# Kernel tuning notes

Hardware: AMD Instinct MI355X
Metric: run time of the kernel (lower is better)

## Reference

```python
import jax, jax.numpy as jnp
import numpy as np

N, E, G = 25600, 409600, 128   # nodes, edges, graphs
IN, H, C = 200, 4, 64          # raw feat dim, heads, hidden_channels
IN2 = 2 * IN                   # after NaN-mask concat
BN_EPS = 1e-5

def _glorot(key, shape):
    lim = float(np.sqrt(6.0 / (shape[0] + shape[-1])))
    return jax.random.uniform(key, shape, jnp.float32, -lim, lim)

def setup_inputs():
    key = jax.random.key(0)
    k = iter(jax.random.split(key, 40))
    inp = {
        "x": jax.random.normal(next(k), (N, IN), jnp.float32),
        "edge_index": jax.random.randint(next(k), (2, E), 0, N, jnp.int32),
        "edge_attr": jax.random.normal(next(k), (E, 1), jnp.float32),
        "batch": jnp.repeat(jnp.arange(G, dtype=jnp.int32), N // G),
    }
    dims = [(IN2, H, C), (H * C, H, C), (H * C, 1, C)]
    for i, (din, h, c) in enumerate(dims):
        inp[f"W{i}"] = _glorot(next(k), (din, h * c))
        inp[f"as{i}"] = _glorot(next(k), (h, c))
        inp[f"ad{i}"] = _glorot(next(k), (h, c))
        inp[f"We{i}"] = _glorot(next(k), (1, h * c))
        inp[f"ae{i}"] = _glorot(next(k), (h, c))
        inp[f"b{i}"] = jnp.zeros((h * c,), jnp.float32)
    inp["bn_g"] = jnp.ones((H * C,), jnp.float32)
    inp["bn_b"] = jnp.zeros((H * C,), jnp.float32)
    inp["bn_m"] = jnp.zeros((H * C,), jnp.float32)
    inp["bn_v"] = jnp.ones((H * C,), jnp.float32)
    inp["cw1"] = _glorot(next(k), (C, C))
    inp["cb1"] = jnp.zeros((C,), jnp.float32)
    inp["cw2"] = _glorot(next(k), (C, 2))
    inp["cb2"] = jnp.zeros((2,), jnp.float32)
    return inp

def _gat(x, src, dst, ea, W, att_s, att_d, We, att_e, b, heads, ch):
    """PyG GATConv (edge_dim=1, add_self_loops=True, fill_value='mean', concat=True)."""
    n = x.shape[0]
    # self-loop edge_attr = mean of incoming edge_attr per destination node
    cnt = jax.ops.segment_sum(jnp.ones((ea.shape[0], 1), ea.dtype), dst, n)
    loop_ea = jax.ops.segment_sum(ea, dst, n) / jnp.maximum(cnt, 1.0)
    idx = jnp.arange(n, dtype=src.dtype)
    src = jnp.concatenate([src, idx])
    dst = jnp.concatenate([dst, idx])
    ea = jnp.concatenate([ea, loop_ea], axis=0)
    h = (x @ W).reshape(n, heads, ch)                      # [N,H,C]
    a_s = jnp.einsum('nhc,hc->nh', h, att_s)
    a_d = jnp.einsum('nhc,hc->nh', h, att_d)
    a_e = jnp.einsum('ehc,hc->eh', (ea @ We).reshape(-1, heads, ch), att_e)
    alpha = jax.nn.leaky_relu(a_s[src] + a_d[dst] + a_e, 0.2)   # [E',H]
    # segment softmax over destination neighborhoods
    m = jax.ops.segment_max(alpha, dst, n)
    ex = jnp.exp(alpha - m[dst])
    z = jax.ops.segment_sum(ex, dst, n)
    alpha = ex / (z[dst] + 1e-16)
    out = jax.ops.segment_sum(h[src] * alpha[:, :, None], dst, n)  # [N,H,C]
    return out.reshape(n, heads * ch) + b

def reference(x, edge_index, edge_attr, batch,
              W0, as0, ad0, We0, ae0, b0,
              W1, as1, ad1, We1, ae1, b1,
              W2, as2, ad2, We2, ae2, b2,
              bn_g, bn_b, bn_m, bn_v, cw1, cb1, cw2, cb2):
    nan_mask = jnp.isnan(x).astype(x.dtype)
    x = jnp.concatenate([jnp.nan_to_num(x), nan_mask], axis=-1)   # [N, 2*IN]
    edge_attr = jnp.nan_to_num(edge_attr)
    src, dst = edge_index[0], edge_index[1]
    for (W, a_s, a_d, We, a_e, b) in [(W0, as0, ad0, We0, ae0, b0),
                                      (W1, as1, ad1, We1, ae1, b1)]:
        x = _gat(x, src, dst, edge_attr, W, a_s, a_d, We, a_e, b, H, C)
        x = (x - bn_m) / jnp.sqrt(bn_v + BN_EPS) * bn_g + bn_b    # eval-mode BN
        x = jax.nn.relu(x)                                        # dropout = identity (eval)
    x = _gat(x, src, dst, edge_attr, W2, as2, ad2, We2, ae2, b2, 1, C)
    # global mean pool over graphs
    cnt = jax.ops.segment_sum(jnp.ones((x.shape[0], 1), x.dtype), batch, G)
    g = jax.ops.segment_sum(x, batch, G) / jnp.maximum(cnt, 1.0)  # [G, C]
    hdn = jax.nn.gelu(g @ cw1 + cb1, approximate=False)
    return hdn @ cw2 + cb2                                        # [G, 2]
```

## Files before the change

kernel.cpp:

```cpp
#include <hip/hip_runtime.h>
#include <hip/hip_bf16.h>

static const int kN  = 25600;
static const int kE  = 409600;
static const int kG  = 128;
static const int kNPG = 200;
static const int kIN = 200;
static const int kIN2 = 400;
static const int kMD = 64;
#define BN_EPS_ 1e-5f

typedef __attribute__((ext_vector_type(8))) short short8;
typedef __attribute__((ext_vector_type(4))) ushort us4;
typedef __attribute__((ext_vector_type(4))) float f32x4;

__device__ __forceinline__ float bu(ushort u) {
  union { float f; unsigned u32; } x; x.u32 = ((unsigned)u) << 16; return x.f;
}
__device__ __forceinline__ ushort f2u(float v) {
  __hip_bfloat16 t = __float2bfloat16(v);
  return *(ushort*)&t;
}
__device__ __forceinline__ float wredSum(float v) {
#pragma unroll
  for (int off = 1; off < 64; off <<= 1) v += __shfl_xor(v, off, 64);
  return v;
}
__device__ __forceinline__ float lrelu(float a) { return (a > 0.f) ? a : 0.2f * a; }

__global__ void k_pre(const float* __restrict__ x, ushort* __restrict__ x2,
                      const float* __restrict__ W0, ushort* __restrict__ Wt0,
                      const float* __restrict__ W1, ushort* __restrict__ Wt1,
                      const float* __restrict__ W2, ushort* __restrict__ Wt2,
                      const float* __restrict__ We0, const float* __restrict__ ae0,
                      const float* __restrict__ We1, const float* __restrict__ ae1,
                      const float* __restrict__ We2, const float* __restrict__ ae2,
                      float* __restrict__ wed,
                      const int* __restrict__ ei, const float* __restrict__ ea,
                      int2* __restrict__ epk, int* __restrict__ deg) {
  int b = blockIdx.x, tid = threadIdx.x;
  if (b < 5000) {
    int i4 = (b * 256 + tid) * 4;
    int n = i4 / kIN, j = i4 - n * kIN;
    float4 v = *(const float4*)&x[i4];
    ushort o0[4], o1[4];
    float vv[4] = {v.x, v.y, v.z, v.w};
#pragma unroll
    for (int q = 0; q < 4; q++) {
      bool bad = (vv[q] != vv[q]);
      o0[q] = f2u(bad ? 0.f : vv[q]);
      o1[q] = f2u(bad ? 1.f : 0.f);
    }
    *(us4*)&x2[(size_t)n * kIN2 + j] = *(us4*)o0;
    *(us4*)&x2[(size_t)n * kIN2 + kIN + j] = *(us4*)o1;
    return;
  }
  int pb = b - 5000;
  if (pb >= 723) {
    int e = (pb - 723) * 256 + tid;
    int d = ei[kE + e];
    int s = ei[e];
    float v = ea[e];
    if (v != v) v = 0.f;
    int slot = atomicAdd(&deg[d], 1);
    if (slot < kMD) {
      int2 rec; rec.x = s; rec.y = __float_as_int(v);
      epk[(size_t)d * kMD + slot] = rec;
    }
    return;
  }
  if (pb >= 720) {
    int l = pb - 720;
    const float* We = (l == 0) ? We0 : (l == 1) ? We1 : We2;
    const float* ae = (l == 0) ? ae0 : (l == 1) ? ae1 : ae2;
    int n = (l == 2) ? 64 : 256;
    float v = (tid < n) ? We[tid] * ae[tid] : 0.f;
    v = wredSum(v);
    if ((tid & 63) == 0 && tid < n) wed[l * 4 + (tid >> 6)] = v;
    return;
  }
  int i = pb * 256 + tid;
  if (i < 102400) {
    int n = i / kIN2, k = i - n * kIN2;
    Wt0[(size_t)n * kIN2 + k] = f2u(W0[(size_t)k * 256 + n]);
  } else if (i < 102400 + 65536) {
    int j = i - 102400;
    int n = j >> 8, k = j & 255;
    Wt1[(size_t)n * 256 + k] = f2u(W1[(size_t)k * 256 + n]);
  } else {
    int j = i - 102400 - 65536;
    int n = j >> 8, k = j & 255;
    Wt2[(size_t)n * 256 + k] = f2u(W2[(size_t)k * 64 + n]);
  }
}

#define GBK 64
#define GPAD 72

template <int BN, int MT>
__global__ __launch_bounds__(256) void k_gemm_f(const ushort* __restrict__ A,
                                                const ushort* __restrict__ Bt,
                                                ushort* __restrict__ C,
                                                const float* __restrict__ as_g,
                                                const float* __restrict__ ad_g,
                                                float* __restrict__ a_sg,
                                                float* __restrict__ a_dg, int K) {
  constexpr int MI = (BN == 256) ? (MT / 16) : 1;
  constexpr int H = (BN == 256) ? 4 : 1;
  __shared__ ushort As[MT * GPAD];
  __shared__ ushort Bs[BN * GPAD];
  int tid = threadIdx.x;
  int lane = tid & 63, w = tid >> 6;
  int l15 = lane & 15, l4 = lane >> 4;
  int row0 = blockIdx.y * MT;
  int wr = (BN == 256) ? 0 : (w * 16);
  int wc = (BN == 256) ? (w * 64) : 0;
  f32x4 acc[MI][4] = {};
  int ach = tid & 7, arow = tid >> 3;

  for (int kt = 0; kt < K; kt += GBK) {
    __syncthreads();
#pragma unroll
    for (int p = 0; p < MT / 32; p++) {
      int r = p * 32 + arow;
      int kg = kt + ach * 8;
      short8 v = {0, 0, 0, 0, 0, 0, 0, 0};
      if (kg < K) v = *(const short8*)&A[(size_t)(row0 + r) * K + kg];
      *(short8*)&As[r * GPAD + ach * 8] = v;
    }
#pragma unroll
    for (int p = 0; p < BN / 32; p++) {
      int r = p * 32 + arow;
      int kg = kt + ach * 8;
      short8 v = {0, 0, 0, 0, 0, 0, 0, 0};
      if (kg < K) v = *(const short8*)&Bt[(size_t)r * K + kg];
      *(short8*)&Bs[r * GPAD + ach * 8] = v;
    }
    __syncthreads();
#pragma unroll
    for (int kk = 0; kk < 2; kk++) {
      short8 af[MI], bf[4];
#pragma unroll
      for (int mi = 0; mi < MI; mi++)
        af[mi] = *(const short8*)&As[(wr + mi * 16 + l15) * GPAD + kk * 32 + l4 * 8];
#pragma unroll
      for (int ni = 0; ni < 4; ni++)
        bf[ni] = *(const short8*)&Bs[(wc + ni * 16 + l15) * GPAD + kk * 32 + l4 * 8];
#pragma unroll
      for (int mi = 0; mi < MI; mi++)
#pragma unroll
        for (int ni = 0; ni < 4; ni++)
          acc[mi][ni] = __builtin_amdgcn_mfma_f32_16x16x32_bf16(af[mi], bf[ni],
                                                                acc[mi][ni], 0, 0, 0);
    }
  }
#pragma unroll
  for (int mi = 0; mi < MI; mi++) {
    int rbase = row0 + wr + mi * 16 + l4 * 4;
#pragma unroll
    for (int ni = 0; ni < 4; ni++) {
      int col = wc + ni * 16 + l15;
#pragma unroll
      for (int r = 0; r < 4; r++)
        C[(size_t)(rbase + r) * BN + col] = f2u(acc[mi][ni][r]);
    }
  }
  float asv[4], adv[4];
#pragma unroll
  for (int ni = 0; ni < 4; ni++) {
    asv[ni] = as_g[wc + ni * 16 + l15];
    adv[ni] = ad_g[wc + ni * 16 + l15];
  }
  int hh = (BN == 256) ? w : 0;
#pragma unroll
  for (int mi = 0; mi < MI; mi++) {
#pragma unroll
    for (int r = 0; r < 4; r++) {
      float ps = 0.f, pd = 0.f;
#pragma unroll
      for (int ni = 0; ni < 4; ni++) {
        ps += acc[mi][ni][r] * asv[ni];
        pd += acc[mi][ni][r] * adv[ni];
      }
#pragma unroll
      for (int off = 1; off < 16; off <<= 1) {
        ps += __shfl_xor(ps, off, 64);
        pd += __shfl_xor(pd, off, 64);
      }
      if (l15 == 0) {
        int row = row0 + wr + mi * 16 + l4 * 4 + r;
        a_sg[row * H + hh] = ps;
        a_dg[row * H + hh] = pd;
      }
    }
  }
}

__global__ __launch_bounds__(256) void k_agg4(
    const ushort* __restrict__ hbuf, const int2* __restrict__ epk,
    const int* __restrict__ deg, const float* __restrict__ a_s,
    const float* __restrict__ a_d, const float* __restrict__ wed,
    const float* __restrict__ bias, const float* __restrict__ bng,
    const float* __restrict__ bnb, const float* __restrict__ bnm,
    const float* __restrict__ bnv, ushort* __restrict__ xout) {
  __shared__ float lds_w[4][kMD][4];
  __shared__ int   lds_s[4][kMD];
  __shared__ float lds_m[4][4][2];
  int tid = threadIdx.x;
  int w = tid >> 6, lane = tid & 63;
  int d = blockIdx.x * 4 + w;
  const int2* rp = &epk[(size_t)d * kMD];
  int dgt = deg[d];
  int dg = min(dgt, kMD);

  int h1 = lane & 3, slot0 = lane >> 2;
  float adh1 = a_d[d * 4 + h1];
  float wdh1 = wed[h1];
  float szp = 0.f, seap = 0.f;
  for (int t = 0; t < dg; t += 16) {
    int slot = t + slot0;
    float wv = 0.f, ev = 0.f;
    if (slot < dg) {
      int2 rec = rp[slot];
      ev = __int_as_float(rec.y);
      float asv = a_s[rec.x * 4 + h1];
      wv = __expf(lrelu(asv + adh1 + ev * wdh1));
      lds_w[w][slot][h1] = wv;
      if (h1 == 0) lds_s[w][slot] = rec.x;
    }
    szp += wv;
    seap += (h1 == 0) ? ev : 0.f;
  }
#pragma unroll
  for (int off = 4; off < 64; off <<= 1) {
    szp  += __shfl_xor(szp, off, 64);
    seap += __shfl_xor(seap, off, 64);
  }
  float sea = __shfl(seap, lane & 0x3C, 64);
  float lea = sea / fmaxf((float)dgt, 1.f);
  float selfw1 = __expf(lrelu(a_s[d * 4 + h1] + adh1 + lea * wdh1));
  float szh = szp + selfw1;
  if (slot0 == 0) {
    lds_m[w][h1][0] = 1.f / (szh + 1e-16f);
    lds_m[w][h1][1] = selfw1;
  }

  int h2 = lane >> 4;
  int c0 = lane * 4;
  float a0 = 0.f, a1 = 0.f, a2 = 0.f, a3 = 0.f;
  int k = 0;
  for (; k + 8 <= dg; k += 8) {
    int s8[8]; float w8[8];
#pragma unroll
    for (int j = 0; j < 8; j++) {
      s8[j] = lds_s[w][k + j];
      w8[j] = lds_w[w][k + j][h2];
    }
    ushort4 v8[8];
#pragma unroll
    for (int j = 0; j < 8; j++)
      v8[j] = *(const ushort4*)&hbuf[(size_t)s8[j] * 256 + c0];
#pragma unroll
    for (int j = 0; j < 8; j++) {
      a0 += w8[j] * bu(v8[j].x); a1 += w8[j] * bu(v8[j].y);
      a2 += w8[j] * bu(v8[j].z); a3 += w8[j] * bu(v8[j].w);
    }
  }
  for (; k < dg; k++) {
    int s0 = lds_s[w][k];
    float w0 = lds_w[w][k][h2];
    ushort4 v0 = *(const ushort4*)&hbuf[(size_t)s0 * 256 + c0];
    a0 += w0 * bu(v0.x); a1 += w0 * bu(v0.y);
    a2 += w0 * bu(v0.z); a3 += w0 * bu(v0.w);
  }
  float winv = lds_m[w][h2][0];
  float sw   = lds_m[w][h2][1];
  {
    ushort4 v0 = *(const ushort4*)&hbuf[(size_t)d * 256 + c0];
    a0 += sw * bu(v0.x); a1 += sw * bu(v0.y);
    a2 += sw * bu(v0.z); a3 += sw * bu(v0.w);
  }

  float4 bi = *(const float4*)&bias[c0];
  a0 = a0 * winv + bi.x; a1 = a1 * winv + bi.y;
  a2 = a2 * winv + bi.z; a3 = a3 * winv + bi.w;
  float4 g4 = *(const float4*)&bng[c0], b4 = *(const float4*)&bnb[c0];
  float4 m4 = *(const float4*)&bnm[c0], v4 = *(const float4*)&bnv[c0];
  a0 = fmaxf((a0 - m4.x) * rsqrtf(v4.x + BN_EPS_) * g4.x + b4.x, 0.f);
  a1 = fmaxf((a1 - m4.y) * rsqrtf(v4.y + BN_EPS_) * g4.y + b4.y, 0.f);
  a2 = fmaxf((a2 - m4.z) * rsqrtf(v4.z + BN_EPS_) * g4.z + b4.z, 0.f);
  a3 = fmaxf((a3 - m4.w) * rsqrtf(v4.w + BN_EPS_) * g4.w + b4.w, 0.f);
  ushort4 o = make_ushort4(f2u(a0), f2u(a1), f2u(a2), f2u(a3));
  *(ushort4*)&xout[(size_t)d * 256 + c0] = o;
}

__global__ __launch_bounds__(256) void k_agg1(
    const ushort* __restrict__ hbuf, const int2* __restrict__ epk,
    const int* __restrict__ deg, const float* __restrict__ a_s,
    const float* __restrict__ a_d, const float* __restrict__ wed,
    const float* __restrict__ bias, float* __restrict__ xout) {
  __shared__ float lds_w[4][kMD];
  __shared__ int   lds_s[4][kMD];
  int tid = threadIdx.x;
  int w = tid >> 6, lane = tid & 63;
  int d = blockIdx.x * 4 + w;
  const int2* rp = &epk[(size_t)d * kMD];
  int dgt = deg[d];
  int dg = min(dgt, kMD);
  float adh = a_d[d];
  float wdh = wed[0];

  float wv = 0.f, ev = 0.f;
  if (lane < dg) {
    int2 rec = rp[lane];
    ev = __int_as_float(rec.y);
    wv = __expf(lrelu(a_s[rec.x] + adh + ev * wdh));
    lds_w[w][lane] = wv;
    lds_s[w][lane] = rec.x;
  }
  float szp = wv, seap = ev;
#pragma unroll
  for (int off = 1; off < 64; off <<= 1) {
    szp  += __shfl_xor(szp, off, 64);
    seap += __shfl_xor(seap, off, 64);
  }
  float lea = seap / fmaxf((float)dgt, 1.f);
  float selfw = __expf(lrelu(a_s[d] + adh + lea * wdh));
  float winv = 1.f / (szp + selfw + 1e-16f);

  float acc = 0.f;
  int k = 0;
  for (; k + 8 <= dg; k += 8) {
    int s8[8]; float w8[8];
#pragma unroll
    for (int j = 0; j < 8; j++) {
      s8[j] = lds_s[w][k + j];
      w8[j] = lds_w[w][k + j];
    }
    ushort v8[8];
#pragma unroll
    for (int j = 0; j < 8; j++) v8[j] = hbuf[(size_t)s8[j] * 64 + lane];
#pragma unroll
    for (int j = 0; j < 8; j++) acc += w8[j] * bu(v8[j]);
  }
  for (; k < dg; k++) {
    acc += lds_w[w][k] * bu(hbuf[(size_t)lds_s[w][k] * 64 + lane]);
  }
  acc += selfw * bu(hbuf[(size_t)d * 64 + lane]);
  acc = acc * winv + bias[lane];
  xout[(size_t)d * 64 + lane] = acc;
}

__global__ void k_poolhead(const float* __restrict__ xin,
                           const float* __restrict__ cw1, const float* __restrict__ cb1,
                           const float* __restrict__ cw2, const float* __restrict__ cb2,
                           float* __restrict__ out) {
  __shared__ float part[4][64];
  __shared__ float gb[64], hb[64];
  int g = blockIdx.x, tid = threadIdx.x;
  int c = tid & 63, w = tid >> 6;
  float acc = 0.f;
  size_t base = (size_t)g * kNPG * 64;
  for (int n = w; n < kNPG; n += 4) acc += xin[base + (size_t)n * 64 + c];
  part[w][c] = acc;
  __syncthreads();
  if (tid < 64) {
    float s = (part[0][c] + part[1][c]) + (part[2][c] + part[3][c]);
    gb[c] = s * (1.f / kNPG);
  }
  __syncthreads();
  if (tid < 64) {
    float s = cb1[c];
#pragma unroll 8
    for (int i = 0; i < 64; i++) s += gb[i] * cw1[i * 64 + c];
    s = 0.5f * s * (1.f + erff(s * 0.70710678118654752f));
    hb[c] = s;
  }
  __syncthreads();
  if (tid < 2) {
    float o = cb2[tid];
    for (int i = 0; i < 64; i++) o += hb[i] * cw2[i * 2 + tid];
    out[g * 2 + tid] = o;
  }
}


extern "C" void kernel_launch(void* const* d_in, const int* in_sizes, int n_in,
                              void* d_out, int out_size, void* d_ws, size_t ws_size,
                              hipStream_t stream) {
  (void)in_sizes; (void)n_in; (void)out_size; (void)ws_size;
  const float* x  = (const float*)d_in[0];
  const int* ei   = (const int*)d_in[1];
  const float* ea = (const float*)d_in[2];
  const float *W[3], *as_[3], *ad_[3], *We[3], *ae[3], *bi[3];
  for (int l = 0; l < 3; l++) {
    W[l]   = (const float*)d_in[4 + l * 6 + 0];
    as_[l] = (const float*)d_in[4 + l * 6 + 1];
    ad_[l] = (const float*)d_in[4 + l * 6 + 2];
    We[l]  = (const float*)d_in[4 + l * 6 + 3];
    ae[l]  = (const float*)d_in[4 + l * 6 + 4];
    bi[l]  = (const float*)d_in[4 + l * 6 + 5];
  }
  const float* bng = (const float*)d_in[22];
  const float* bnb = (const float*)d_in[23];
  const float* bnm = (const float*)d_in[24];
  const float* bnv = (const float*)d_in[25];
  const float* cw1 = (const float*)d_in[26];
  const float* cb1 = (const float*)d_in[27];
  const float* cw2 = (const float*)d_in[28];
  const float* cb2 = (const float*)d_in[29];

  char* p = (char*)d_ws;
  auto alloc = [&](size_t bytes) -> void* {
    void* r = (void*)p;
    p += (bytes + 255) & ~(size_t)255;
    return r;
  };
  ushort* x2b   = (ushort*)alloc((size_t)kN * kIN2 * 2);
  ushort* hbufb = (ushort*)alloc((size_t)kN * 256 * 2);
  ushort* xbA   = (ushort*)alloc((size_t)kN * 256 * 2);
  ushort* xbB   = (ushort*)alloc((size_t)kN * 256 * 2);
  float*  fbuf  = (float*)alloc((size_t)kN * 64 * 4);
  ushort* Wt0   = (ushort*)alloc((size_t)kIN2 * 256 * 2);
  ushort* Wt1   = (ushort*)alloc((size_t)256 * 256 * 2);
  ushort* Wt2   = (ushort*)alloc((size_t)256 * 64 * 2);
  float* a_s    = (float*)alloc((size_t)kN * 4 * 4);
  float* a_d    = (float*)alloc((size_t)kN * 4 * 4);
  int2* epk     = (int2*)alloc((size_t)kN * kMD * 8);
  float* wed    = (float*)alloc(256);
  int* deg      = (int*)alloc((size_t)kN * 4);

  hipMemsetAsync(deg, 0, (size_t)kN * 4, stream);
  k_pre<<<5000 + 720 + 3 + 1600, 256, 0, stream>>>(
      x, x2b, W[0], Wt0, W[1], Wt1, W[2], Wt2, We[0], ae[0], We[1], ae[1],
      We[2], ae[2], wed, ei, ea, epk, deg);
  dim3 gg64m(1, kN / 64);
  k_gemm_f<256, 64><<<gg64m, 256, 0, stream>>>(x2b, Wt0, hbufb, as_[0], ad_[0],
                                               a_s, a_d, kIN2);
  k_agg4<<<kN / 4, 256, 0, stream>>>(hbufb, epk, deg, a_s, a_d,
                                     &wed[0], bi[0], bng, bnb, bnm, bnv, xbA);
  k_gemm_f<256, 64><<<gg64m, 256, 0, stream>>>(xbA, Wt1, hbufb, as_[1], ad_[1],
                                               a_s, a_d, 256);
  k_agg4<<<kN / 4, 256, 0, stream>>>(hbufb, epk, deg, a_s, a_d,
                                     &wed[4], bi[1], bng, bnb, bnm, bnv, xbB);
  dim3 gg64(1, kN / 64);
  k_gemm_f<64, 64><<<gg64, 256, 0, stream>>>(xbB, Wt2, hbufb, as_[2], ad_[2],
                                             a_s, a_d, 256);
  k_agg1<<<kN / 4, 256, 0, stream>>>(hbufb, epk, deg, a_s, a_d,
                                     &wed[8], bi[2], fbuf);
  k_poolhead<<<kG, 256, 0, stream>>>(fbuf, cw1, cb1, cw2, cb2, (float*)d_out);
}
```

Before: 299.3 us.

## Use direct global-to-LDS loads with XOR swizzle, fuse pooling into aggregation

```diff
diff --git a/kernel.cpp b/kernel.cpp
--- a/kernel.cpp
+++ b/kernel.cpp
@@ -7,6 +7,7 @@
 static const int kNPG = 200;
 static const int kIN = 200;
 static const int kIN2 = 400;
+static const int kK0 = 448;
 static const int kMD = 64;
 #define BN_EPS_ 1e-5f
 
@@ -27,6 +28,10 @@
   return v;
 }
 __device__ __forceinline__ float lrelu(float a) { return (a > 0.f) ? a : 0.2f * a; }
+
+#define GLOAD16(g, l) __builtin_amdgcn_global_load_lds( \
+    (const __attribute__((address_space(1))) unsigned int*)(g), \
+    (__attribute__((address_space(3))) unsigned int*)(l), 16, 0, 0)
 
 __global__ void k_pre(const float* __restrict__ x, ushort* __restrict__ x2,
                       const float* __restrict__ W0, ushort* __restrict__ Wt0,
@@ -51,11 +56,26 @@
       o0[q] = f2u(bad ? 0.f : vv[q]);
       o1[q] = f2u(bad ? 1.f : 0.f);
     }
-    *(us4*)&x2[(size_t)n * kIN2 + j] = *(us4*)o0;
-    *(us4*)&x2[(size_t)n * kIN2 + kIN + j] = *(us4*)o1;
+    *(us4*)&x2[(size_t)n * kK0 + j] = *(us4*)o0;
+    *(us4*)&x2[(size_t)n * kK0 + kIN + j] = *(us4*)o1;
     return;
   }
   int pb = b - 5000;
+  if (pb >= 2323) {
+    int idx = (pb - 2323) * 256 + tid;
+    short8 z = {0, 0, 0, 0, 0, 0, 0, 0};
+    if (idx < 153600) {
+      int row = idx / 6, c = idx - row * 6;
+      *(short8*)&x2[(size_t)row * kK0 + kIN2 + c * 8] = z;
+    } else {
+      int j = idx - 153600;
+      if (j < 1536) {
+        int row = j / 6, c = j - row * 6;
+        *(short8*)&Wt0[(size_t)row * kK0 + kIN2 + c * 8] = z;
+      }
+    }
+    return;
+  }
   if (pb >= 723) {
     int e = (pb - 723) * 256 + tid;
     int d = ei[kE + e];
@@ -82,7 +102,7 @@
   int i = pb * 256 + tid;
   if (i < 102400) {
     int n = i / kIN2, k = i - n * kIN2;
-    Wt0[(size_t)n * kIN2 + k] = f2u(W0[(size_t)k * 256 + n]);
+    Wt0[(size_t)n * kK0 + k] = f2u(W0[(size_t)k * 256 + n]);
   } else if (i < 102400 + 65536) {
     int j = i - 102400;
     int n = j >> 8, k = j & 255;
@@ -93,9 +113,6 @@
     Wt2[(size_t)n * 256 + k] = f2u(W2[(size_t)k * 64 + n]);
   }
 }
-
-#define GBK 64
-#define GPAD 72
 
 template <int BN, int MT>
 __global__ __launch_bounds__(256) void k_gemm_f(const ushort* __restrict__ A,
@@ -107,8 +124,8 @@
                                                 float* __restrict__ a_dg, int K) {
   constexpr int MI = (BN == 256) ? (MT / 16) : 1;
   constexpr int H = (BN == 256) ? 4 : 1;
-  __shared__ ushort As[MT * GPAD];
-  __shared__ ushort Bs[BN * GPAD];
+  __shared__ ushort As[MT * 64];
+  __shared__ ushort Bs[BN * 64];
   int tid = threadIdx.x;
   int lane = tid & 63, w = tid >> 6;
   int l15 = lane & 15, l4 = lane >> 4;
@@ -116,36 +133,39 @@
   int wr = (BN == 256) ? 0 : (w * 16);
   int wc = (BN == 256) ? (w * 64) : 0;
   f32x4 acc[MI][4] = {};
-  int ach = tid & 7, arow = tid >> 3;
-
-  for (int kt = 0; kt < K; kt += GBK) {
+  int srow = lane >> 3;
+  int schunk = lane & 7;
+
+  for (int kt = 0; kt < K; kt += 64) {
     __syncthreads();
 #pragma unroll
-    for (int p = 0; p < MT / 32; p++) {
-      int r = p * 32 + arow;
-      int kg = kt + ach * 8;
-      short8 v = {0, 0, 0, 0, 0, 0, 0, 0};
-      if (kg < K) v = *(const short8*)&A[(size_t)(row0 + r) * K + kg];
-      *(short8*)&As[r * GPAD + ach * 8] = v;
-    }
-#pragma unroll
-    for (int p = 0; p < BN / 32; p++) {
-      int r = p * 32 + arow;
-      int kg = kt + ach * 8;
-      short8 v = {0, 0, 0, 0, 0, 0, 0, 0};
-      if (kg < K) v = *(const short8*)&Bt[(size_t)r * K + kg];
-      *(short8*)&Bs[r * GPAD + ach * 8] = v;
+    for (int i = 0; i < MT / 32; i++) {
+      int ra = w * (MT / 4) + i * 8;
+      int r = ra + srow;
+      GLOAD16(&A[(size_t)(row0 + r) * K + kt + ((schunk ^ (r & 7)) * 8)],
+              &As[ra * 64]);
+    }
+#pragma unroll
+    for (int i = 0; i < BN / 32; i++) {
+      int rb = w * (BN / 4) + i * 8;
+      int r = rb + srow;
+      GLOAD16(&Bt[(size_t)r * K + kt + ((schunk ^ (r & 7)) * 8)],
+              &Bs[rb * 64]);
     }
     __syncthreads();
 #pragma unroll
     for (int kk = 0; kk < 2; kk++) {
       short8 af[MI], bf[4];
 #pragma unroll
-      for (int mi = 0; mi < MI; mi++)
-        af[mi] = *(const short8*)&As[(wr + mi * 16 + l15) * GPAD + kk * 32 + l4 * 8];
-#pragma unroll
-      for (int ni = 0; ni < 4; ni++)
-        bf[ni] = *(const short8*)&Bs[(wc + ni * 16 + l15) * GPAD + kk * 32 + l4 * 8];
+      for (int mi = 0; mi < MI; mi++) {
+        int r = wr + mi * 16 + l15;
+        af[mi] = *(const short8*)&As[r * 64 + ((kk * 32 + l4 * 8) ^ ((r & 7) * 8))];
+      }
+#pragma unroll
+      for (int ni = 0; ni < 4; ni++) {
+        int r = wc + ni * 16 + l15;
+        bf[ni] = *(const short8*)&Bs[r * 64 + ((kk * 32 + l4 * 8) ^ ((r & 7) * 8))];
+      }
 #pragma unroll
       for (int mi = 0; mi < MI; mi++)
 #pragma unroll
@@ -247,8 +267,26 @@
 
   int h2 = lane >> 4;
   int c0 = lane * 4;
+  ushort4 vself = *(const ushort4*)&hbuf[(size_t)d * 256 + c0];
   float a0 = 0.f, a1 = 0.f, a2 = 0.f, a3 = 0.f;
   int k = 0;
+  for (; k + 16 <= dg; k += 16) {
+    int s16[16]; float w16[16];
+#pragma unroll
+    for (int j = 0; j < 16; j++) {
+      s16[j] = lds_s[w][k + j];
+      w16[j] = lds_w[w][k + j][h2];
+    }
+    ushort4 v16[16];
+#pragma unroll
+    for (int j = 0; j < 16; j++)
+      v16[j] = *(const ushort4*)&hbuf[(size_t)s16[j] * 256 + c0];
+#pragma unroll
+    for (int j = 0; j < 16; j++) {
+      a0 += w16[j] * bu(v16[j].x); a1 += w16[j] * bu(v16[j].y);
+      a2 += w16[j] * bu(v16[j].z); a3 += w16[j] * bu(v16[j].w);
+    }
+  }
   for (; k + 8 <= dg; k += 8) {
     int s8[8]; float w8[8];
 #pragma unroll
@@ -275,11 +313,8 @@
   }
   float winv = lds_m[w][h2][0];
   float sw   = lds_m[w][h2][1];
-  {
-    ushort4 v0 = *(const ushort4*)&hbuf[(size_t)d * 256 + c0];
-    a0 += sw * bu(v0.x); a1 += sw * bu(v0.y);
-    a2 += sw * bu(v0.z); a3 += sw * bu(v0.w);
-  }
+  a0 += sw * bu(vself.x); a1 += sw * bu(vself.y);
+  a2 += sw * bu(vself.z); a3 += sw * bu(vself.w);
 
   float4 bi = *(const float4*)&bias[c0];
   a0 = a0 * winv + bi.x; a1 = a1 * winv + bi.y;
@@ -298,9 +333,10 @@
     const ushort* __restrict__ hbuf, const int2* __restrict__ epk,
     const int* __restrict__ deg, const float* __restrict__ a_s,
     const float* __restrict__ a_d, const float* __restrict__ wed,
-    const float* __restrict__ bias, float* __restrict__ xout) {
+    float* __restrict__ gsum) {
   __shared__ float lds_w[4][kMD];
   __shared__ int   lds_s[4][kMD];
+  __shared__ float part[4][64];
   int tid = threadIdx.x;
   int w = tid >> 6, lane = tid & 63;
   int d = blockIdx.x * 4 + w;
@@ -328,8 +364,22 @@
   float selfw = __expf(lrelu(a_s[d] + adh + lea * wdh));
   float winv = 1.f / (szp + selfw + 1e-16f);
 
+  float vselff = bu(hbuf[(size_t)d * 64 + lane]);
   float acc = 0.f;
   int k = 0;
+  for (; k + 16 <= dg; k += 16) {
+    int s16[16]; float w16[16];
+#pragma unroll
+    for (int j = 0; j < 16; j++) {
+      s16[j] = lds_s[w][k + j];
+      w16[j] = lds_w[w][k + j];
+    }
+    ushort v16[16];
+#pragma unroll
+    for (int j = 0; j < 16; j++) v16[j] = hbuf[(size_t)s16[j] * 64 + lane];
+#pragma unroll
+    for (int j = 0; j < 16; j++) acc += w16[j] * bu(v16[j]);
+  }
   for (; k + 8 <= dg; k += 8) {
     int s8[8]; float w8[8];
 #pragma unroll
@@ -346,41 +396,36 @@
   for (; k < dg; k++) {
     acc += lds_w[w][k] * bu(hbuf[(size_t)lds_s[w][k] * 64 + lane]);
   }
-  acc += selfw * bu(hbuf[(size_t)d * 64 + lane]);
-  acc = acc * winv + bias[lane];
-  xout[(size_t)d * 64 + lane] = acc;
-}
-
-__global__ void k_poolhead(const float* __restrict__ xin,
-                           const float* __restrict__ cw1, const float* __restrict__ cb1,
-                           const float* __restrict__ cw2, const float* __restrict__ cb2,
-                           float* __restrict__ out) {
-  __shared__ float part[4][64];
+  acc += selfw * vselff;
+  acc = acc * winv;
+
+  part[w][lane] = acc;
+  __syncthreads();
+  if (w == 0) {
+    float s = (part[0][lane] + part[1][lane]) + (part[2][lane] + part[3][lane]);
+    int g = (blockIdx.x * 4) / kNPG;
+    atomicAdd(&gsum[g * 64 + lane], s);
+  }
+}
+
+__global__ void k_head(const float* __restrict__ gsum, const float* __restrict__ bias,
+                       const float* __restrict__ cw1, const float* __restrict__ cb1,
+                       const float* __restrict__ cw2, const float* __restrict__ cb2,
+                       float* __restrict__ out) {
   __shared__ float gb[64], hb[64];
-  int g = blockIdx.x, tid = threadIdx.x;
-  int c = tid & 63, w = tid >> 6;
-  float acc = 0.f;
-  size_t base = (size_t)g * kNPG * 64;
-  for (int n = w; n < kNPG; n += 4) acc += xin[base + (size_t)n * 64 + c];
-  part[w][c] = acc;
+  int g = blockIdx.x, c = threadIdx.x;
+  gb[c] = gsum[g * 64 + c] * (1.f / kNPG) + bias[c];
   __syncthreads();
-  if (tid < 64) {
-    float s = (part[0][c] + part[1][c]) + (part[2][c] + part[3][c]);
-    gb[c] = s * (1.f / kNPG);
-  }
+  float s = cb1[c];
+#pragma unroll 8
+  for (int i = 0; i < 64; i++) s += gb[i] * cw1[i * 64 + c];
+  s = 0.5f * s * (1.f + erff(s * 0.70710678118654752f));
+  hb[c] = s;
   __syncthreads();
-  if (tid < 64) {
-    float s = cb1[c];
-#pragma unroll 8
-    for (int i = 0; i < 64; i++) s += gb[i] * cw1[i * 64 + c];
-    s = 0.5f * s * (1.f + erff(s * 0.70710678118654752f));
-    hb[c] = s;
-  }
-  __syncthreads();
-  if (tid < 2) {
-    float o = cb2[tid];
-    for (int i = 0; i < 64; i++) o += hb[i] * cw2[i * 2 + tid];
-    out[g * 2 + tid] = o;
+  if (c < 2) {
+    float o = cb2[c];
+    for (int i = 0; i < 64; i++) o += hb[i] * cw2[i * 2 + c];
+    out[g * 2 + c] = o;
   }
 }
 
@@ -416,12 +461,11 @@
     p += (bytes + 255) & ~(size_t)255;
     return r;
   };
-  ushort* x2b   = (ushort*)alloc((size_t)kN * kIN2 * 2);
+  ushort* x2b   = (ushort*)alloc((size_t)kN * kK0 * 2);
   ushort* hbufb = (ushort*)alloc((size_t)kN * 256 * 2);
   ushort* xbA   = (ushort*)alloc((size_t)kN * 256 * 2);
   ushort* xbB   = (ushort*)alloc((size_t)kN * 256 * 2);
-  float*  fbuf  = (float*)alloc((size_t)kN * 64 * 4);
-  ushort* Wt0   = (ushort*)alloc((size_t)kIN2 * 256 * 2);
+  ushort* Wt0   = (ushort*)alloc((size_t)kK0 * 256 * 2);
   ushort* Wt1   = (ushort*)alloc((size_t)256 * 256 * 2);
   ushort* Wt2   = (ushort*)alloc((size_t)256 * 64 * 2);
   float* a_s    = (float*)alloc((size_t)kN * 4 * 4);
@@ -429,14 +473,15 @@
   int2* epk     = (int2*)alloc((size_t)kN * kMD * 8);
   float* wed    = (float*)alloc(256);
   int* deg      = (int*)alloc((size_t)kN * 4);
-
-  hipMemsetAsync(deg, 0, (size_t)kN * 4, stream);
-  k_pre<<<5000 + 720 + 3 + 1600, 256, 0, stream>>>(
+  float* gsum   = (float*)alloc((size_t)kG * 64 * 4);
+
+  hipMemsetAsync(deg, 0, (size_t)kN * 4 + (size_t)kG * 64 * 4, stream);
+  k_pre<<<5000 + 2929, 256, 0, stream>>>(
       x, x2b, W[0], Wt0, W[1], Wt1, W[2], Wt2, We[0], ae[0], We[1], ae[1],
       We[2], ae[2], wed, ei, ea, epk, deg);
   dim3 gg64m(1, kN / 64);
   k_gemm_f<256, 64><<<gg64m, 256, 0, stream>>>(x2b, Wt0, hbufb, as_[0], ad_[0],
-                                               a_s, a_d, kIN2);
+                                               a_s, a_d, kK0);
   k_agg4<<<kN / 4, 256, 0, stream>>>(hbufb, epk, deg, a_s, a_d,
                                      &wed[0], bi[0], bng, bnb, bnm, bnv, xbA);
   k_gemm_f<256, 64><<<gg64m, 256, 0, stream>>>(xbA, Wt1, hbufb, as_[1], ad_[1],
@@ -446,7 +491,6 @@
   dim3 gg64(1, kN / 64);
   k_gemm_f<64, 64><<<gg64, 256, 0, stream>>>(xbB, Wt2, hbufb, as_[2], ad_[2],
                                              a_s, a_d, 256);
-  k_agg1<<<kN / 4, 256, 0, stream>>>(hbufb, epk, deg, a_s, a_d,
-                                     &wed[8], bi[2], fbuf);
-  k_poolhead<<<kG, 256, 0, stream>>>(fbuf, cw1, cb1, cw2, cb2, (float*)d_out);
-}
+  k_agg1<<<kN / 4, 256, 0, stream>>>(hbufb, epk, deg, a_s, a_d, &wed[8], gsum);
+  k_head<<<kG, 64, 0, stream>>>(gsum, bi[2], cw1, cb1, cw2, cb2, (float*)d_out);
+}
```

New measurement: 292.8 us. -2.2%, faster.
